# Performance work log

Measured on AMD Instinct MI355X. Metric: run time of the kernel, lower is better.

The kernel has to match this reference:

```python
import jax, jax.numpy as jnp
import numpy as np

TOP_K = 2
NUM_EXPERTS = 8


def setup_inputs() -> dict:
    key = jax.random.key(0)
    ks = jax.random.split(key, 9)
    B, S, N, H = 1, 8, 1024, 512
    E, I_moe, I_sh = NUM_EXPERTS, 2048 // TOP_K, 2048
    s = 0.02
    return {
        "hidden_states": jax.random.normal(ks[0], (B, S, N, H), dtype=jnp.float32),
        "gate_w": jax.random.normal(ks[1], (E, H), dtype=jnp.float32) * s,
        "expert_w1": jax.random.normal(ks[2], (E, I_moe, H), dtype=jnp.float32) * s,
        "expert_w2": jax.random.normal(ks[3], (E, H, I_moe), dtype=jnp.float32) * s,
        "expert_w3": jax.random.normal(ks[4], (E, I_moe, H), dtype=jnp.float32) * s,
        "shared_w1": jax.random.normal(ks[5], (I_sh, H), dtype=jnp.float32) * s,
        "shared_w2": jax.random.normal(ks[6], (H, I_sh), dtype=jnp.float32) * s,
        "shared_w3": jax.random.normal(ks[7], (I_sh, H), dtype=jnp.float32) * s,
        "shared_gate_w": jax.random.normal(ks[8], (1, H), dtype=jnp.float32) * s,
    }


def reference(hidden_states, gate_w, expert_w1, expert_w2, expert_w3,
              shared_w1, shared_w2, shared_w3, shared_gate_w):
    B, S, N, H = hidden_states.shape
    x = hidden_states.reshape(-1, H)                       # [T, H], T = B*S*N

    # Router: softmax in fp32, then top-k (norm_topk_prob=False).
    router_logits = x @ gate_w.T                           # [T, E]
    probs = jax.nn.softmax(router_logits.astype(jnp.float32), axis=-1)
    top_w, top_i = jax.lax.top_k(probs, TOP_K)             # [T, k]
    # Combine weight per (token, expert): zero for unselected experts.
    combine = jnp.sum(top_w[..., None] * jax.nn.one_hot(top_i, NUM_EXPERTS, dtype=probs.dtype), axis=1)
    combine = combine.astype(x.dtype)                      # [T, E]

    # Routed experts (SwiGLU FFN per expert), evaluated densely and masked
    # by the sparse combine weights (same math as gather/scatter dispatch).
    h1 = jnp.einsum('th,eih->tei', x, expert_w1)           # [T, E, I_moe]
    h3 = jnp.einsum('th,eih->tei', x, expert_w3)
    h = jax.nn.silu(h1) * h3
    expert_out = jnp.einsum('tei,ehi->teh', h, expert_w2)  # [T, E, H]
    moe_out = jnp.einsum('te,teh->th', combine, expert_out)

    # Shared expert with sigmoid gate.
    sh = (jax.nn.silu(x @ shared_w1.T) * (x @ shared_w3.T)) @ shared_w2.T
    sgate = jax.nn.sigmoid(x @ shared_gate_w.T)            # [T, 1]
    out = moe_out + sgate * sh

    return out.reshape(B, S, N, H), router_logits
```

## Files before the change

kernel.cpp:

```cpp
#include <hip/hip_runtime.h>
#include <hip/hip_bf16.h>
#include <stdint.h>
#include <math.h>

typedef __bf16 bf16;
typedef bf16 bf16x8 __attribute__((ext_vector_type(8)));
typedef bf16 bf16x4 __attribute__((ext_vector_type(4)));
typedef float f32x4 __attribute__((ext_vector_type(4)));
typedef unsigned int u32;

#define TOKENS 8192
#define HD 512
#define NE 8
#define IM 1024
#define ISH 2048
#define CAP 2560

__device__ __forceinline__ void gld16(const void* g, void* l) {
  __builtin_amdgcn_global_load_lds(
      (const __attribute__((address_space(1))) u32*)g,
      (__attribute__((address_space(3))) u32*)l, 16, 0, 0);
}

#define RT_BLOCKS (TOKENS / 4)
#define CVT_BLOCKS 3840
#define CVT_STRIDE (CVT_BLOCKS * 256)
#define F4_E  (NE * IM * HD / 4)
#define F4_S  (ISH * HD / 4)
#define F4_C1 (F4_E)
#define F4_C2 (F4_C1 + F4_E)
#define F4_C3 (F4_C2 + F4_S)
#define F4_C4 (F4_C3 + F4_S)
#define F4_C5 (F4_C4 + F4_E)
#define F4_TOT (F4_C5 + F4_S)

__launch_bounds__(256)
__global__ void router_cvt_k(const float* __restrict__ x, const float* __restrict__ gw,
                             const float* __restrict__ sgw, float* __restrict__ logits,
                             float* __restrict__ sgate, int* __restrict__ topi,
                             float* __restrict__ topw, int* __restrict__ counts,
                             bf16* __restrict__ xb,
                             const float* __restrict__ e1, const float* __restrict__ e3,
                             const float* __restrict__ s1, const float* __restrict__ s3,
                             const float* __restrict__ e2, const float* __restrict__ s2,
                             bf16* __restrict__ wdst) {
  if (blockIdx.x >= RT_BLOCKS) {
    int idx = (blockIdx.x - RT_BLOCKS) * 256 + threadIdx.x;
#pragma unroll
    for (int it = 0; it < 4; it++, idx += CVT_STRIDE) {
      const float* s; int off;
      if (idx < F4_C1)      { s = e1; off = idx; }
      else if (idx < F4_C2) { s = e3; off = idx - F4_C1; }
      else if (idx < F4_C3) { s = s1; off = idx - F4_C2; }
      else if (idx < F4_C4) { s = s3; off = idx - F4_C3; }
      else if (idx < F4_C5) { s = e2; off = idx - F4_C4; }
      else                  { s = s2; off = idx - F4_C5; }
      const float4 v = ((const float4*)s)[off];
      bf16x4 o;
      o.x = (bf16)v.x; o.y = (bf16)v.y; o.z = (bf16)v.z; o.w = (bf16)v.w;
      ((bf16x4*)wdst)[idx] = o;
    }
    return;
  }
  if (blockIdx.x == 0 && threadIdx.x < NE) counts[threadIdx.x] = 0;
  __shared__ float gws[9][512];
  for (int i = threadIdx.x; i < 9 * 512; i += 256) {
    int r = i >> 9, c = i & 511;
    float v = (r < 8) ? gw[i] : sgw[c];
    gws[r][((c & 7) << 6) | (c >> 3)] = v;
  }
  __syncthreads();
  int wave = threadIdx.x >> 6, lane = threadIdx.x & 63;
  int t = blockIdx.x * 4 + wave;
  const float* xp = x + (size_t)t * HD + lane * 8;
  float4 va = *(const float4*)xp;
  float4 vb = *(const float4*)(xp + 4);
  float xv[8] = {va.x, va.y, va.z, va.w, vb.x, vb.y, vb.z, vb.w};
  {
    bf16x8 xo;
#pragma unroll
    for (int j = 0; j < 8; j++) xo[j] = (bf16)xv[j];
    *(bf16x8*)(xb + (size_t)t * HD + lane * 8) = xo;
  }
  float acc[9];
#pragma unroll
  for (int e = 0; e < 9; e++) {
    float a = 0.f;
#pragma unroll
    for (int j = 0; j < 8; j++) a = fmaf(xv[j], gws[e][j * 64 + lane], a);
    acc[e] = a;
  }
#pragma unroll
  for (int off = 32; off > 0; off >>= 1) {
#pragma unroll
    for (int e = 0; e < 9; e++) acc[e] += __shfl_down(acc[e], off);
  }
  if (lane == 0) {
    float mx = acc[0];
#pragma unroll
    for (int e = 1; e < 8; e++) mx = fmaxf(mx, acc[e]);
    float p[8], sum = 0.f;
#pragma unroll
    for (int e = 0; e < 8; e++) { p[e] = expf(acc[e] - mx); sum += p[e]; }
    float inv = 1.f / sum;
    int i0 = 0; float b0 = p[0];
#pragma unroll
    for (int e = 1; e < 8; e++) if (p[e] > b0) { b0 = p[e]; i0 = e; }
    int i1 = -1; float b1 = -1.f;
#pragma unroll
    for (int e = 0; e < 8; e++) if (e != i0 && p[e] > b1) { b1 = p[e]; i1 = e; }
#pragma unroll
    for (int e = 0; e < 8; e++) logits[(size_t)t * 8 + e] = acc[e];
    topi[2 * t] = i0; topi[2 * t + 1] = i1;
    topw[2 * t] = b0 * inv; topw[2 * t + 1] = b1 * inv;
    sgate[t] = 1.f / (1.f + expf(-acc[8]));
  }
}

__launch_bounds__(256)
__global__ void dispatch_k(const int* __restrict__ topi, const float* __restrict__ topw,
                           int* __restrict__ counts, int* __restrict__ tok,
                           float* __restrict__ wl, int* __restrict__ pos) {
  __shared__ int lcnt[NE];
  __shared__ int lbase[NE];
  int tid = threadIdx.x;
  if (tid < NE) lcnt[tid] = 0;
  __syncthreads();
  int t = blockIdx.x * 256 + tid;
  int e0 = topi[2 * t], e1 = topi[2 * t + 1];
  float w0 = topw[2 * t], w1 = topw[2 * t + 1];
  int r0 = atomicAdd(&lcnt[e0], 1);
  int r1 = atomicAdd(&lcnt[e1], 1);
  __syncthreads();
  if (tid < NE) lbase[tid] = atomicAdd(&counts[tid], lcnt[tid]);
  __syncthreads();
  int p0 = lbase[e0] + r0;
  int p1 = lbase[e1] + r1;
  if (p0 < CAP) { tok[e0 * CAP + p0] = t; wl[e0 * CAP + p0] = w0; }
  if (p1 < CAP) { tok[e1 * CAP + p1] = t; wl[e1 * CAP + p1] = w1; }
  pos[2 * t]     = (p0 < CAP) ? e0 * CAP + p0 : -1;
  pos[2 * t + 1] = (p1 < CAP) ? e1 * CAP + p1 : -1;
}

__launch_bounds__(256, 4)
__global__ void gemm1_k(const bf16* __restrict__ X, const int* __restrict__ tokl,
                        const int* __restrict__ counts,
                        const bf16* __restrict__ e1w, const bf16* __restrict__ e3w,
                        const bf16* __restrict__ s1w, const bf16* __restrict__ s3w,
                        bf16* __restrict__ hmoe, bf16* __restrict__ hsh) {
  int g = blockIdx.y * 16 + blockIdx.x;
  int xcd = g & 7, i = g >> 3;
  int y, bx;
  if (i < 320) { y = xcd * 20 + (i >> 4); bx = i & 15; }
  else { int s = i - 320; y = 160 + xcd * 16 + (s >> 4); bx = s & 15; }

  const bf16 *W1, *W3;
  bf16* Hout;
  const int* tl = nullptr;
  int cnt = 0, m0, n0, N;
  bool gather;
  if (y < 160) {
    int e = y / 20, mt = y % 20;
    cnt = min(counts[e], CAP);
    if (mt * 128 >= cnt) return;
    gather = true;
    tl = tokl + e * CAP;
    W1 = e1w + (size_t)e * IM * HD;
    W3 = e3w + (size_t)e * IM * HD;
    Hout = hmoe + (size_t)e * CAP * IM;
    N = IM; m0 = mt * 128; n0 = bx * 64;
  } else {
    int s = y - 160;
    gather = false;
    W1 = s1w; W3 = s3w; Hout = hsh; N = ISH;
    m0 = (s >> 1) * 128;
    n0 = ((s & 1) * 16 + bx) * 64;
  }

  __shared__ __align__(16) bf16 As[2][128 * 32];
  __shared__ __align__(16) bf16 B1s[2][64 * 32];
  __shared__ __align__(16) bf16 B3s[2][64 * 32];

  int tid = threadIdx.x;
  int sr = tid >> 2;
  int colb = (((tid & 3) ^ ((sr >> 1) & 3)) * 16);
  int ar0, ar1;
  if (gather) {
    ar0 = tl[min(m0 + sr, cnt - 1)];
    ar1 = tl[min(m0 + 64 + sr, cnt - 1)];
  } else { ar0 = m0 + sr; ar1 = m0 + 64 + sr; }
  const char* apa = (const char*)(X + (size_t)ar0 * HD) + colb;
  const char* apb = (const char*)(X + (size_t)ar1 * HD) + colb;
  const char* bp1 = (const char*)(W1 + (size_t)(n0 + sr) * HD) + colb;
  const char* bp3 = (const char*)(W3 + (size_t)(n0 + sr) * HD) + colb;
  char* lA0a = (char*)&As[0][0] + tid * 16;
  char* lA0b = (char*)&As[1][0] + tid * 16;
  char* lA1a = (char*)&As[0][0] + 4096 + tid * 16;
  char* lA1b = (char*)&As[1][0] + 4096 + tid * 16;
  char* lB1a = (char*)&B1s[0][0] + tid * 16;
  char* lB1b = (char*)&B1s[1][0] + tid * 16;
  char* lB3a = (char*)&B3s[0][0] + tid * 16;
  char* lB3b = (char*)&B3s[1][0] + tid * 16;

  int wid = tid >> 6, lane = tid & 63;
  int wm = (wid >> 1) * 64, wn = (wid & 1) * 32;
  int lrow = lane & 15, lq = lane >> 4;
  int sl = (lq ^ ((lrow >> 1) & 3)) * 8;

  f32x4 acc1[4][2] = {};
  f32x4 acc3[4][2] = {};

  for (int kb = 0; kb < 1024; kb += 128) {
    __syncthreads();
    gld16(apa + kb, lA0a);      gld16(apa + kb + 64, lA0b);
    gld16(apb + kb, lA1a);      gld16(apb + kb + 64, lA1b);
    gld16(bp1 + kb, lB1a);      gld16(bp1 + kb + 64, lB1b);
    gld16(bp3 + kb, lB3a);      gld16(bp3 + kb + 64, lB3b);
    __syncthreads();
#pragma unroll
    for (int ks = 0; ks < 2; ks++) {
      bf16x8 a[4], b1[2], b3[2];
#pragma unroll
      for (int i2 = 0; i2 < 4; i2++)
        a[i2] = *(const bf16x8*)&As[ks][(wm + i2 * 16 + lrow) * 32 + sl];
#pragma unroll
      for (int j = 0; j < 2; j++) {
        b1[j] = *(const bf16x8*)&B1s[ks][(wn + j * 16 + lrow) * 32 + sl];
        b3[j] = *(const bf16x8*)&B3s[ks][(wn + j * 16 + lrow) * 32 + sl];
      }
#pragma unroll
      for (int i2 = 0; i2 < 4; i2++)
#pragma unroll
        for (int j = 0; j < 2; j++) {
          acc1[i2][j] = __builtin_amdgcn_mfma_f32_16x16x32_bf16(a[i2], b1[j], acc1[i2][j], 0, 0, 0);
          acc3[i2][j] = __builtin_amdgcn_mfma_f32_16x16x32_bf16(a[i2], b3[j], acc3[i2][j], 0, 0, 0);
        }
    }
  }

#pragma unroll
  for (int i2 = 0; i2 < 4; i2++)
#pragma unroll
    for (int r = 0; r < 4; r++) {
      int row = m0 + wm + i2 * 16 + lq * 4 + r;
#pragma unroll
      for (int j = 0; j < 2; j++) {
        float v1 = acc1[i2][j][r], v3 = acc3[i2][j][r];
        float hv = v1 / (1.f + __expf(-v1)) * v3;
        Hout[(size_t)row * N + (n0 + wn + j * 16 + lrow)] = (bf16)hv;
      }
    }
}

__launch_bounds__(256, 4)
__global__ void gemm2_k(const bf16* __restrict__ hmoe, const bf16* __restrict__ hsh,
                        const bf16* __restrict__ e2w, const bf16* __restrict__ s2w,
                        const float* __restrict__ wll, const int* __restrict__ counts,
                        bf16* __restrict__ yslot, bf16* __restrict__ ysh) {
  const bf16 *Hin, *W2;
  const float* wlp = nullptr;
  bf16* Yout;
  int cnt = 0, m0, K;
  bool weighted;
  int y = blockIdx.y;
  if (y < 64) {
    weighted = false;
    Hin = hsh; W2 = s2w; Yout = ysh; K = ISH; m0 = y * 128;
  } else {
    int e = (y - 64) / 20, mt = (y - 64) % 20;
    cnt = min(counts[e], CAP);
    if (mt * 128 >= cnt) return;
    weighted = true;
    Hin = hmoe + (size_t)e * CAP * IM;
    W2 = e2w + (size_t)e * HD * IM;
    wlp = wll + e * CAP;
    Yout = yslot + (size_t)e * CAP * HD;
    K = IM; m0 = mt * 128;
  }
  int n0 = blockIdx.x * 128;

  __shared__ __align__(16) bf16 As[2][128 * 32];
  __shared__ __align__(16) bf16 Bs[2][128 * 32];

  int tid = threadIdx.x;
  int sr = tid >> 2;
  int colb = (((tid & 3) ^ ((sr >> 1) & 3)) * 16);
  const char* apa = (const char*)(Hin + (size_t)(m0 + sr) * K) + colb;
  const char* apb = (const char*)(Hin + (size_t)(m0 + 64 + sr) * K) + colb;
  const char* bpa = (const char*)(W2 + (size_t)(n0 + sr) * K) + colb;
  const char* bpb = (const char*)(W2 + (size_t)(n0 + 64 + sr) * K) + colb;
  char* lA0a = (char*)&As[0][0] + tid * 16;
  char* lA0b = (char*)&As[1][0] + tid * 16;
  char* lA1a = (char*)&As[0][0] + 4096 + tid * 16;
  char* lA1b = (char*)&As[1][0] + 4096 + tid * 16;
  char* lB0a = (char*)&Bs[0][0] + tid * 16;
  char* lB0b = (char*)&Bs[1][0] + tid * 16;
  char* lB1a = (char*)&Bs[0][0] + 4096 + tid * 16;
  char* lB1b = (char*)&Bs[1][0] + 4096 + tid * 16;

  int wid = tid >> 6, lane = tid & 63;
  int wm = (wid >> 1) * 64, wn = (wid & 1) * 64;
  int lrow = lane & 15, lq = lane >> 4;
  int sl = (lq ^ ((lrow >> 1) & 3)) * 8;

  f32x4 acc[4][4] = {};

  for (int kb = 0; kb < K * 2; kb += 128) {
    __syncthreads();
    gld16(apa + kb, lA0a);      gld16(apa + kb + 64, lA0b);
    gld16(apb + kb, lA1a);      gld16(apb + kb + 64, lA1b);
    gld16(bpa + kb, lB0a);      gld16(bpa + kb + 64, lB0b);
    gld16(bpb + kb, lB1a);      gld16(bpb + kb + 64, lB1b);
    __syncthreads();
#pragma unroll
    for (int ks = 0; ks < 2; ks++) {
      bf16x8 a[4], b[4];
#pragma unroll
      for (int i2 = 0; i2 < 4; i2++) {
        a[i2] = *(const bf16x8*)&As[ks][(wm + i2 * 16 + lrow) * 32 + sl];
        b[i2] = *(const bf16x8*)&Bs[ks][(wn + i2 * 16 + lrow) * 32 + sl];
      }
#pragma unroll
      for (int i2 = 0; i2 < 4; i2++)
#pragma unroll
        for (int j = 0; j < 4; j++)
          acc[i2][j] = __builtin_amdgcn_mfma_f32_16x16x32_bf16(a[i2], b[j], acc[i2][j], 0, 0, 0);
    }
  }

#pragma unroll
  for (int i2 = 0; i2 < 4; i2++)
#pragma unroll
    for (int r = 0; r < 4; r++) {
      int row = m0 + wm + i2 * 16 + lq * 4 + r;
      float w = weighted ? ((row < cnt) ? wlp[row] : 0.f) : 1.f;
      bf16* op = Yout + (size_t)row * HD;
#pragma unroll
      for (int j = 0; j < 4; j++)
        op[n0 + wn + j * 16 + lrow] = (bf16)(w * acc[i2][j][r]);
    }
}

__launch_bounds__(256)
__global__ void combine_k(const bf16* __restrict__ yslot, const bf16* __restrict__ ysh,
                          const int* __restrict__ pos, const float* __restrict__ sgate,
                          float* __restrict__ out) {
  int wave = threadIdx.x >> 6, lane = threadIdx.x & 63;
  int t = blockIdx.x * 4 + wave;
  int p0 = pos[2 * t], p1 = pos[2 * t + 1];
  float g = sgate[t];
  int col = lane * 8;
  float acc[8];
  {
    const bf16x8 s = *(const bf16x8*)(ysh + (size_t)t * HD + col);
#pragma unroll
    for (int i = 0; i < 8; i++) acc[i] = g * (float)s[i];
  }
  if (p0 >= 0) {
    const bf16x8 v = *(const bf16x8*)(yslot + (size_t)p0 * HD + col);
#pragma unroll
    for (int i = 0; i < 8; i++) acc[i] += (float)v[i];
  }
  if (p1 >= 0) {
    const bf16x8 v = *(const bf16x8*)(yslot + (size_t)p1 * HD + col);
#pragma unroll
    for (int i = 0; i < 8; i++) acc[i] += (float)v[i];
  }
  float* op = out + (size_t)t * HD + col;
#pragma unroll
  for (int i = 0; i < 8; i++) op[i] = acc[i];
}

extern "C" void kernel_launch(void* const* d_in, const int* in_sizes, int n_in,
                              void* d_out, int out_size, void* d_ws, size_t ws_size,
                              hipStream_t stream) {
  const float* x   = (const float*)d_in[0];
  const float* gw  = (const float*)d_in[1];
  const float* ew1 = (const float*)d_in[2];
  const float* ew2 = (const float*)d_in[3];
  const float* ew3 = (const float*)d_in[4];
  const float* sw1 = (const float*)d_in[5];
  const float* sw2 = (const float*)d_in[6];
  const float* sw3 = (const float*)d_in[7];
  const float* sgw = (const float*)d_in[8];
  float* out = (float*)d_out;
  float* logits = out + (size_t)TOKENS * HD;

  char* w = (char*)d_ws;
  bf16* xb  = (bf16*)w; w += (size_t)TOKENS * HD * 2;
  bf16* e1b = (bf16*)w; w += (size_t)NE * IM * HD * 2;
  bf16* e3b = (bf16*)w; w += (size_t)NE * IM * HD * 2;
  bf16* s1b = (bf16*)w; w += (size_t)ISH * HD * 2;
  bf16* s3b = (bf16*)w; w += (size_t)ISH * HD * 2;
  bf16* e2b = (bf16*)w; w += (size_t)NE * HD * IM * 2;
  bf16* s2b = (bf16*)w; w += (size_t)HD * ISH * 2;
  float* sgate = (float*)w; w += TOKENS * 4;
  int*   topi  = (int*)w;   w += TOKENS * 2 * 4;
  float* topw  = (float*)w; w += TOKENS * 2 * 4;
  int*   counts = (int*)w;  w += 256;
  int*   tok   = (int*)w;   w += NE * CAP * 4;
  float* wl    = (float*)w; w += NE * CAP * 4;
  int*   pos   = (int*)w;   w += TOKENS * 2 * 4;
  bf16* hmoe = (bf16*)w; w += (size_t)NE * CAP * IM * 2;
  bf16* hsh  = (bf16*)w; w += (size_t)TOKENS * ISH * 2;
  bf16* yslot = xb;
  bf16* ysh   = (bf16*)((char*)xb + (size_t)NE * CAP * HD * 2);

  hipLaunchKernelGGL(router_cvt_k, dim3(RT_BLOCKS + CVT_BLOCKS), dim3(256), 0, stream,
                     x, gw, sgw, logits, sgate, topi, topw, counts, xb,
                     ew1, ew3, sw1, sw3, ew2, sw2, e1b);
  hipLaunchKernelGGL(dispatch_k, dim3(TOKENS / 256), dim3(256), 0, stream,
                     topi, topw, counts, tok, wl, pos);
  hipLaunchKernelGGL(gemm1_k, dim3(16, 160 + 128), dim3(256), 0, stream,
                     xb, tok, counts, e1b, e3b, s1b, s3b, hmoe, hsh);
  hipLaunchKernelGGL(gemm2_k, dim3(4, 64 + 160), dim3(256), 0, stream,
                     hmoe, hsh, e2b, s2b, wl, counts, yslot, ysh);
  hipLaunchKernelGGL(combine_k, dim3(TOKENS / 4), dim3(256), 0, stream,
                     yslot, ysh, pos, sgate, out);
}
```

Baseline: 266.8 us.

## Double-buffer LDS staging in both expert GEMM kernels to overlap loads with MFMA

The K loops of gemm1 and gemm2 now use ping-pong LDS buffers. Before, both K-halves were loaded, the block synchronised, and then both were computed. Now the global-to-LDS load for the next 32-wide K slice is issued before computing on the current slice, with a barrier between stages. This is meant to hide global load latency behind the MFMA work, at the cost of an extra barrier per K slice. The loops are also kept rolled (unroll 1), which limits instruction scheduling across iterations.

New measurement: 290.9 us. 9.0% more time.

```diff
diff --git a/kernel.cpp b/kernel.cpp
--- a/kernel.cpp
+++ b/kernel.cpp
@@ -193,14 +193,12 @@
   const char* apb = (const char*)(X + (size_t)ar1 * HD) + colb;
   const char* bp1 = (const char*)(W1 + (size_t)(n0 + sr) * HD) + colb;
   const char* bp3 = (const char*)(W3 + (size_t)(n0 + sr) * HD) + colb;
-  char* lA0a = (char*)&As[0][0] + tid * 16;
-  char* lA0b = (char*)&As[1][0] + tid * 16;
-  char* lA1a = (char*)&As[0][0] + 4096 + tid * 16;
-  char* lA1b = (char*)&As[1][0] + 4096 + tid * 16;
-  char* lB1a = (char*)&B1s[0][0] + tid * 16;
-  char* lB1b = (char*)&B1s[1][0] + tid * 16;
-  char* lB3a = (char*)&B3s[0][0] + tid * 16;
-  char* lB3b = (char*)&B3s[1][0] + tid * 16;
+  char* lA0  = (char*)&As[0][0]  + tid * 16;
+  char* lA1  = (char*)&As[1][0]  + tid * 16;
+  char* lB10 = (char*)&B1s[0][0] + tid * 16;
+  char* lB11 = (char*)&B1s[1][0] + tid * 16;
+  char* lB30 = (char*)&B3s[0][0] + tid * 16;
+  char* lB31 = (char*)&B3s[1][0] + tid * 16;
 
   int wid = tid >> 6, lane = tid & 63;
   int wm = (wid >> 1) * 64, wn = (wid & 1) * 32;
@@ -210,33 +208,36 @@
   f32x4 acc1[4][2] = {};
   f32x4 acc3[4][2] = {};
 
-  for (int kb = 0; kb < 1024; kb += 128) {
+#define STG1(c, k) { \
+    gld16(apa + (k) * 64, ((c) ? lA1 : lA0)); \
+    gld16(apb + (k) * 64, ((c) ? lA1 : lA0) + 4096); \
+    gld16(bp1 + (k) * 64, ((c) ? lB11 : lB10)); \
+    gld16(bp3 + (k) * 64, ((c) ? lB31 : lB30)); }
+#define CMP1(c) { \
+    bf16x8 a[4], b1[2], b3[2]; \
+    _Pragma("unroll") for (int i2 = 0; i2 < 4; i2++) \
+      a[i2] = *(const bf16x8*)&As[c][(wm + i2 * 16 + lrow) * 32 + sl]; \
+    _Pragma("unroll") for (int j = 0; j < 2; j++) { \
+      b1[j] = *(const bf16x8*)&B1s[c][(wn + j * 16 + lrow) * 32 + sl]; \
+      b3[j] = *(const bf16x8*)&B3s[c][(wn + j * 16 + lrow) * 32 + sl]; } \
+    _Pragma("unroll") for (int i2 = 0; i2 < 4; i2++) \
+    _Pragma("unroll") for (int j = 0; j < 2; j++) { \
+      acc1[i2][j] = __builtin_amdgcn_mfma_f32_16x16x32_bf16(a[i2], b1[j], acc1[i2][j], 0, 0, 0); \
+      acc3[i2][j] = __builtin_amdgcn_mfma_f32_16x16x32_bf16(a[i2], b3[j], acc3[i2][j], 0, 0, 0); } }
+
+  STG1(0, 0);
+  __syncthreads();
+#pragma unroll 1
+  for (int k = 0; k < 8; ++k) {
+    STG1(1, 2 * k + 1);
+    CMP1(0);
     __syncthreads();
-    gld16(apa + kb, lA0a);      gld16(apa + kb + 64, lA0b);
-    gld16(apb + kb, lA1a);      gld16(apb + kb + 64, lA1b);
-    gld16(bp1 + kb, lB1a);      gld16(bp1 + kb + 64, lB1b);
-    gld16(bp3 + kb, lB3a);      gld16(bp3 + kb + 64, lB3b);
+    if (k < 7) STG1(0, 2 * k + 2);
+    CMP1(1);
     __syncthreads();
-#pragma unroll
-    for (int ks = 0; ks < 2; ks++) {
-      bf16x8 a[4], b1[2], b3[2];
-#pragma unroll
-      for (int i2 = 0; i2 < 4; i2++)
-        a[i2] = *(const bf16x8*)&As[ks][(wm + i2 * 16 + lrow) * 32 + sl];
-#pragma unroll
-      for (int j = 0; j < 2; j++) {
-        b1[j] = *(const bf16x8*)&B1s[ks][(wn + j * 16 + lrow) * 32 + sl];
-        b3[j] = *(const bf16x8*)&B3s[ks][(wn + j * 16 + lrow) * 32 + sl];
-      }
-#pragma unroll
-      for (int i2 = 0; i2 < 4; i2++)
-#pragma unroll
-        for (int j = 0; j < 2; j++) {
-          acc1[i2][j] = __builtin_amdgcn_mfma_f32_16x16x32_bf16(a[i2], b1[j], acc1[i2][j], 0, 0, 0);
-          acc3[i2][j] = __builtin_amdgcn_mfma_f32_16x16x32_bf16(a[i2], b3[j], acc3[i2][j], 0, 0, 0);
-        }
-    }
-  }
+  }
+#undef STG1
+#undef CMP1
 
 #pragma unroll
   for (int i2 = 0; i2 < 4; i2++)
@@ -289,14 +290,10 @@
   const char* apb = (const char*)(Hin + (size_t)(m0 + 64 + sr) * K) + colb;
   const char* bpa = (const char*)(W2 + (size_t)(n0 + sr) * K) + colb;
   const char* bpb = (const char*)(W2 + (size_t)(n0 + 64 + sr) * K) + colb;
-  char* lA0a = (char*)&As[0][0] + tid * 16;
-  char* lA0b = (char*)&As[1][0] + tid * 16;
-  char* lA1a = (char*)&As[0][0] + 4096 + tid * 16;
-  char* lA1b = (char*)&As[1][0] + 4096 + tid * 16;
-  char* lB0a = (char*)&Bs[0][0] + tid * 16;
-  char* lB0b = (char*)&Bs[1][0] + tid * 16;
-  char* lB1a = (char*)&Bs[0][0] + 4096 + tid * 16;
-  char* lB1b = (char*)&Bs[1][0] + 4096 + tid * 16;
+  char* lA0 = (char*)&As[0][0] + tid * 16;
+  char* lA1 = (char*)&As[1][0] + tid * 16;
+  char* lB0 = (char*)&Bs[0][0] + tid * 16;
+  char* lB1 = (char*)&Bs[1][0] + tid * 16;
 
   int wid = tid >> 6, lane = tid & 63;
   int wm = (wid >> 1) * 64, wn = (wid & 1) * 64;
@@ -305,28 +302,34 @@
 
   f32x4 acc[4][4] = {};
 
-  for (int kb = 0; kb < K * 2; kb += 128) {
+#define STG2(c, k) { \
+    gld16(apa + (k) * 64, ((c) ? lA1 : lA0)); \
+    gld16(apb + (k) * 64, ((c) ? lA1 : lA0) + 4096); \
+    gld16(bpa + (k) * 64, ((c) ? lB1 : lB0)); \
+    gld16(bpb + (k) * 64, ((c) ? lB1 : lB0) + 4096); }
+#define CMP2(c) { \
+    bf16x8 a[4], b[4]; \
+    _Pragma("unroll") for (int i2 = 0; i2 < 4; i2++) { \
+      a[i2] = *(const bf16x8*)&As[c][(wm + i2 * 16 + lrow) * 32 + sl]; \
+      b[i2] = *(const bf16x8*)&Bs[c][(wn + i2 * 16 + lrow) * 32 + sl]; } \
+    _Pragma("unroll") for (int i2 = 0; i2 < 4; i2++) \
+    _Pragma("unroll") for (int j = 0; j < 4; j++) \
+      acc[i2][j] = __builtin_amdgcn_mfma_f32_16x16x32_bf16(a[i2], b[j], acc[i2][j], 0, 0, 0); }
+
+  int nk = K / 64;
+  STG2(0, 0);
+  __syncthreads();
+#pragma unroll 1
+  for (int k = 0; k < nk; ++k) {
+    STG2(1, 2 * k + 1);
+    CMP2(0);
     __syncthreads();
-    gld16(apa + kb, lA0a);      gld16(apa + kb + 64, lA0b);
-    gld16(apb + kb, lA1a);      gld16(apb + kb + 64, lA1b);
-    gld16(bpa + kb, lB0a);      gld16(bpa + kb + 64, lB0b);
-    gld16(bpb + kb, lB1a);      gld16(bpb + kb + 64, lB1b);
+    if (k < nk - 1) STG2(0, 2 * k + 2);
+    CMP2(1);
     __syncthreads();
-#pragma unroll
-    for (int ks = 0; ks < 2; ks++) {
-      bf16x8 a[4], b[4];
-#pragma unroll
-      for (int i2 = 0; i2 < 4; i2++) {
-        a[i2] = *(const bf16x8*)&As[ks][(wm + i2 * 16 + lrow) * 32 + sl];
-        b[i2] = *(const bf16x8*)&Bs[ks][(wn + i2 * 16 + lrow) * 32 + sl];
-      }
-#pragma unroll
-      for (int i2 = 0; i2 < 4; i2++)
-#pragma unroll
-        for (int j = 0; j < 4; j++)
-          acc[i2][j] = __builtin_amdgcn_mfma_f32_16x16x32_bf16(a[i2], b[j], acc[i2][j], 0, 0, 0);
-    }
-  }
+  }
+#undef STG2
+#undef CMP2
 
 #pragma unroll
   for (int i2 = 0; i2 < 4; i2++)
```

## Triple-buffer gemm1 LDS loads with async prefetch and vmcnt-based waits

Applied to the files above, without the earlier changes.

Replaces gemm1's load-then-compute double-slice loop with a three-stage ring of LDS buffers. Each 32-wide K slice is prefetched two steps ahead via global_load_lds, and completion is gated by explicit s_waitcnt vmcnt counts plus raw s_barrier. The aim is to overlap global-to-LDS traffic with MFMA work instead of stalling on full __syncthreads around every load. In exchange LDS use grows by half and launch bounds drop from 4 to 3 blocks per CU, which lowers occupancy. Correctness also depends on the hand-counted vmcnt values and on there being no LDS write-after-read hazards.

After: 284.6 us. 6.7% more time.

```diff
diff --git a/kernel.cpp b/kernel.cpp
--- a/kernel.cpp
+++ b/kernel.cpp
@@ -142,7 +142,7 @@
   pos[2 * t + 1] = (p1 < CAP) ? e1 * CAP + p1 : -1;
 }
 
-__launch_bounds__(256, 4)
+__launch_bounds__(256, 3)
 __global__ void gemm1_k(const bf16* __restrict__ X, const int* __restrict__ tokl,
                         const int* __restrict__ counts,
                         const bf16* __restrict__ e1w, const bf16* __restrict__ e3w,
@@ -177,9 +177,9 @@
     n0 = ((s & 1) * 16 + bx) * 64;
   }
 
-  __shared__ __align__(16) bf16 As[2][128 * 32];
-  __shared__ __align__(16) bf16 B1s[2][64 * 32];
-  __shared__ __align__(16) bf16 B3s[2][64 * 32];
+  __shared__ __align__(16) bf16 As[3][128 * 32];
+  __shared__ __align__(16) bf16 B1s[3][64 * 32];
+  __shared__ __align__(16) bf16 B3s[3][64 * 32];
 
   int tid = threadIdx.x;
   int sr = tid >> 2;
@@ -193,14 +193,9 @@
   const char* apb = (const char*)(X + (size_t)ar1 * HD) + colb;
   const char* bp1 = (const char*)(W1 + (size_t)(n0 + sr) * HD) + colb;
   const char* bp3 = (const char*)(W3 + (size_t)(n0 + sr) * HD) + colb;
-  char* lA0a = (char*)&As[0][0] + tid * 16;
-  char* lA0b = (char*)&As[1][0] + tid * 16;
-  char* lA1a = (char*)&As[0][0] + 4096 + tid * 16;
-  char* lA1b = (char*)&As[1][0] + 4096 + tid * 16;
-  char* lB1a = (char*)&B1s[0][0] + tid * 16;
-  char* lB1b = (char*)&B1s[1][0] + tid * 16;
-  char* lB3a = (char*)&B3s[0][0] + tid * 16;
-  char* lB3b = (char*)&B3s[1][0] + tid * 16;
+  char* lA  = (char*)&As[0][0]  + tid * 16;
+  char* lB1 = (char*)&B1s[0][0] + tid * 16;
+  char* lB3 = (char*)&B3s[0][0] + tid * 16;
 
   int wid = tid >> 6, lane = tid & 63;
   int wm = (wid >> 1) * 64, wn = (wid & 1) * 32;
@@ -210,33 +205,40 @@
   f32x4 acc1[4][2] = {};
   f32x4 acc3[4][2] = {};
 
-  for (int kb = 0; kb < 1024; kb += 128) {
-    __syncthreads();
-    gld16(apa + kb, lA0a);      gld16(apa + kb + 64, lA0b);
-    gld16(apb + kb, lA1a);      gld16(apb + kb + 64, lA1b);
-    gld16(bp1 + kb, lB1a);      gld16(bp1 + kb + 64, lB1b);
-    gld16(bp3 + kb, lB3a);      gld16(bp3 + kb + 64, lB3b);
-    __syncthreads();
-#pragma unroll
-    for (int ks = 0; ks < 2; ks++) {
-      bf16x8 a[4], b1[2], b3[2];
-#pragma unroll
-      for (int i2 = 0; i2 < 4; i2++)
-        a[i2] = *(const bf16x8*)&As[ks][(wm + i2 * 16 + lrow) * 32 + sl];
-#pragma unroll
-      for (int j = 0; j < 2; j++) {
-        b1[j] = *(const bf16x8*)&B1s[ks][(wn + j * 16 + lrow) * 32 + sl];
-        b3[j] = *(const bf16x8*)&B3s[ks][(wn + j * 16 + lrow) * 32 + sl];
-      }
-#pragma unroll
-      for (int i2 = 0; i2 < 4; i2++)
-#pragma unroll
-        for (int j = 0; j < 2; j++) {
-          acc1[i2][j] = __builtin_amdgcn_mfma_f32_16x16x32_bf16(a[i2], b1[j], acc1[i2][j], 0, 0, 0);
-          acc3[i2][j] = __builtin_amdgcn_mfma_f32_16x16x32_bf16(a[i2], b3[j], acc3[i2][j], 0, 0, 0);
-        }
-    }
-  }
+#define STG(bi, k) { \
+    gld16(apa + (k) * 64, lA + (bi) * 8192); \
+    gld16(apb + (k) * 64, lA + (bi) * 8192 + 4096); \
+    gld16(bp1 + (k) * 64, lB1 + (bi) * 4096); \
+    gld16(bp3 + (k) * 64, lB3 + (bi) * 4096); }
+#define CMP(bi) { \
+    bf16x8 a[4], b1v[2], b3v[2]; \
+    _Pragma("unroll") for (int i2 = 0; i2 < 4; i2++) \
+      a[i2] = *(const bf16x8*)&As[bi][(wm + i2 * 16 + lrow) * 32 + sl]; \
+    _Pragma("unroll") for (int j = 0; j < 2; j++) { \
+      b1v[j] = *(const bf16x8*)&B1s[bi][(wn + j * 16 + lrow) * 32 + sl]; \
+      b3v[j] = *(const bf16x8*)&B3s[bi][(wn + j * 16 + lrow) * 32 + sl]; } \
+    _Pragma("unroll") for (int i2 = 0; i2 < 4; i2++) \
+    _Pragma("unroll") for (int j = 0; j < 2; j++) { \
+      acc1[i2][j] = __builtin_amdgcn_mfma_f32_16x16x32_bf16(a[i2], b1v[j], acc1[i2][j], 0, 0, 0); \
+      acc3[i2][j] = __builtin_amdgcn_mfma_f32_16x16x32_bf16(a[i2], b3v[j], acc3[i2][j], 0, 0, 0); } }
+#define SLICE(s) { \
+    if ((s) < 14) STG(((s) + 2) % 3, (s) + 2); \
+    CMP((s) % 3); \
+    if ((s) == 14)     { asm volatile("s_waitcnt vmcnt(0)" ::: "memory"); } \
+    else if ((s) < 14) { asm volatile("s_waitcnt vmcnt(4)" ::: "memory"); } \
+    if ((s) < 15) __builtin_amdgcn_s_barrier(); }
+
+  STG(0, 0); STG(1, 1);
+  asm volatile("s_waitcnt vmcnt(4)" ::: "memory");
+  __builtin_amdgcn_s_barrier();
+
+  SLICE(0)  SLICE(1)  SLICE(2)  SLICE(3)
+  SLICE(4)  SLICE(5)  SLICE(6)  SLICE(7)
+  SLICE(8)  SLICE(9)  SLICE(10) SLICE(11)
+  SLICE(12) SLICE(13) SLICE(14) SLICE(15)
+#undef STG
+#undef CMP
+#undef SLICE
 
 #pragma unroll
   for (int i2 = 0; i2 < 4; i2++)
```
